# Optimization experiments

Measured on AMD Instinct MI355X. Metric: run time of the kernel, lower is better.

## Reference

```python
import jax, jax.numpy as jnp
import numpy as np

N_NODES = 100000

def _spmm(edge_index, edge_weight, support):
    # out[row] += w * support[col]  (COO spmm)
    row, col = edge_index[0], edge_index[1]
    msgs = edge_weight[:, None] * support[col]          # [E, D] gather
    return jax.ops.segment_sum(msgs, row, num_segments=N_NODES)

def setup_inputs() -> dict:
    key = jax.random.key(0)
    ks = jax.random.split(key, 7)
    N, E, F_IN, H1, H2 = N_NODES, 1600000, 256, 128, 64
    x = jax.random.normal(ks[0], (N, F_IN), dtype=jnp.float32)
    edge_index = jax.random.randint(ks[1], (2, E), 0, N, dtype=jnp.int64)
    edge_weight = jax.random.uniform(ks[2], (E,), dtype=jnp.float32)
    s1 = 1.0 / np.sqrt(H1)
    s2 = 1.0 / np.sqrt(H2)
    W1 = jax.random.uniform(ks[3], (F_IN, H1), jnp.float32, -s1, s1)
    b1 = jax.random.uniform(ks[4], (H1,), jnp.float32, -s1, s1)
    W2 = jax.random.uniform(ks[5], (H1, H2), jnp.float32, -s2, s2)
    b2 = jax.random.uniform(ks[6], (H2,), jnp.float32, -s2, s2)
    return {"x": x, "edge_index": edge_index, "edge_weight": edge_weight,
            "W1": W1, "b1": b1, "W2": W2, "b2": b2}

def reference(x, edge_index, edge_weight, W1, b1, W2, b2):
    # GraphConvolution 1: dense mm -> spmm -> bias, then ReLU
    h = _spmm(edge_index, edge_weight, x @ W1) + b1
    h = jax.nn.relu(h)
    # Dropout is identity in eval mode (training=False)
    # GraphConvolution 2
    out = _spmm(edge_index, edge_weight, h @ W2) + b2
    return out
```

## Files before the change

kernel.cpp:

```cpp
#include <hip/hip_runtime.h>


constexpr int F_IN = 256, H1 = 128, H2 = 64;
constexpr int BSH = 9;
constexpr int CHUNK = 8192;
constexpr float QS = 5.5f / 127.f;
constexpr float QSI = 127.f / 5.5f;

typedef __attribute__((ext_vector_type(8))) short bf16x8;
typedef __attribute__((ext_vector_type(8))) unsigned short u16x8;
typedef __attribute__((ext_vector_type(4))) float f32x4;

__device__ inline float bf2f(unsigned short u) { return __uint_as_float((unsigned)u << 16); }
__device__ inline unsigned short f2bf(float f) {
    unsigned u = __float_as_uint(f);
    u += 0x7fff + ((u >> 16) & 1);
    return (unsigned short)(u >> 16);
}

__device__ inline signed char f2i8(float f) {
    int q = __float2int_rn(f * QSI);
    q = q > 127 ? 127 : (q < -127 ? -127 : q);
    return (signed char)q;
}

__device__ inline void gload16(const void* g, void* l) {
    __builtin_amdgcn_global_load_lds((const __attribute__((address_space(1))) void*)g,
                                     (__attribute__((address_space(3))) void*)l, 16, 0, 0);
}

__global__ __launch_bounds__(256) void k_count(const int* __restrict__ ei, int E, int N,
                                               int* __restrict__ cnt, int NWG, int nbuck) {
    __shared__ int lh[256];
    int wg = blockIdx.x, t = threadIdx.x;
    if (t < nbuck) lh[t] = 0;
    __syncthreads();
    int base = wg * CHUNK;
#pragma unroll
    for (int j = 0; j < CHUNK / 1024; ++j) {
        int e = base + j * 1024 + t * 4;
        if (e + 3 < E) {
            int4 r4 = *(const int4*)&ei[e];
            unsigned r0 = (unsigned)r4.x, r1 = (unsigned)r4.y;
            unsigned r2 = (unsigned)r4.z, r3 = (unsigned)r4.w;
            if (r0 < (unsigned)N) atomicAdd(&lh[r0 >> BSH], 1);
            if (r1 < (unsigned)N) atomicAdd(&lh[r1 >> BSH], 1);
            if (r2 < (unsigned)N) atomicAdd(&lh[r2 >> BSH], 1);
            if (r3 < (unsigned)N) atomicAdd(&lh[r3 >> BSH], 1);
        } else {
            for (int k = 0; k < 4; ++k) {
                int ee = e + k;
                if (ee < E) {
                    unsigned r = (unsigned)ei[ee];
                    if (r < (unsigned)N) atomicAdd(&lh[r >> BSH], 1);
                }
            }
        }
    }
    __syncthreads();
    if (t < nbuck) cnt[t * NWG + wg] = lh[t];
}

__global__ __launch_bounds__(256) void k_rowscan(int* __restrict__ cnt, int NWG,
                                                 int* __restrict__ btot) {
    __shared__ int s[256];
    int b = blockIdx.x, t = threadIdx.x;
    int v = (t < NWG) ? cnt[b * NWG + t] : 0;
    s[t] = v;
    __syncthreads();
    for (int off = 1; off < 256; off <<= 1) {
        int tv = (t >= off) ? s[t - off] : 0;
        __syncthreads();
        s[t] += tv;
        __syncthreads();
    }
    if (t < NWG) cnt[b * NWG + t] = s[t] - v;
    if (t == 255) btot[b] = s[255];
}

__global__ __launch_bounds__(256) void k_bscan(const int* __restrict__ btot, int nbuck,
                                               int* __restrict__ bbase) {
    __shared__ int s[256];
    int t = threadIdx.x;
    int v = (t < nbuck) ? btot[t] : 0;
    s[t] = v;
    __syncthreads();
    for (int off = 1; off < 256; off <<= 1) {
        int tv = (t >= off) ? s[t - off] : 0;
        __syncthreads();
        s[t] += tv;
        __syncthreads();
    }
    if (t < nbuck) bbase[t] = s[t] - v;
    if (t == nbuck - 1) bbase[nbuck] = s[t];
}

__global__ __launch_bounds__(256) void k_place(const int* __restrict__ ei,
                                               const float* __restrict__ ew, int E, int N,
                                               const int* __restrict__ cnt,
                                               const int* __restrict__ bbase,
                                               int NWG, int nbuck,
                                               int2* __restrict__ tmp) {
    __shared__ int cur[256];
    int wg = blockIdx.x, t = threadIdx.x;
    if (t < nbuck) cur[t] = cnt[t * NWG + wg] + bbase[t];
    __syncthreads();
    int base = wg * CHUNK;
#pragma unroll
    for (int j = 0; j < CHUNK / 1024; ++j) {
        int e = base + j * 1024 + t * 4;
        if (e + 3 < E) {
            int4 r4 = *(const int4*)&ei[e];
            int4 c4 = *(const int4*)&ei[E + e];
            float4 w4 = *(const float4*)&ew[e];
            unsigned r, c;
            r = (unsigned)r4.x; c = (unsigned)c4.x;
            if (r < (unsigned)N && c < (unsigned)N) {
                int p = atomicAdd(&cur[r >> BSH], 1);
                tmp[p] = make_int2((int)(((r & 511u) << 17) | c), __float_as_int(w4.x));
            }
            r = (unsigned)r4.y; c = (unsigned)c4.y;
            if (r < (unsigned)N && c < (unsigned)N) {
                int p = atomicAdd(&cur[r >> BSH], 1);
                tmp[p] = make_int2((int)(((r & 511u) << 17) | c), __float_as_int(w4.y));
            }
            r = (unsigned)r4.z; c = (unsigned)c4.z;
            if (r < (unsigned)N && c < (unsigned)N) {
                int p = atomicAdd(&cur[r >> BSH], 1);
                tmp[p] = make_int2((int)(((r & 511u) << 17) | c), __float_as_int(w4.z));
            }
            r = (unsigned)r4.w; c = (unsigned)c4.w;
            if (r < (unsigned)N && c < (unsigned)N) {
                int p = atomicAdd(&cur[r >> BSH], 1);
                tmp[p] = make_int2((int)(((r & 511u) << 17) | c), __float_as_int(w4.w));
            }
        } else {
            for (int k = 0; k < 4; ++k) {
                int ee = e + k;
                if (ee < E) {
                    unsigned r = (unsigned)ei[ee];
                    unsigned c = (unsigned)ei[E + ee];
                    if (r < (unsigned)N && c < (unsigned)N) {
                        int p = atomicAdd(&cur[r >> BSH], 1);
                        tmp[p] = make_int2((int)(((r & 511u) << 17) | c),
                                           __float_as_int(ew[ee]));
                    }
                }
            }
        }
    }
}

__global__ __launch_bounds__(1024) void k_bfinal(const int2* __restrict__ tmp,
                                                 const int* __restrict__ bbase,
                                                 int* __restrict__ row_ptr,
                                                 int2* __restrict__ cw, int N, int nbuck) {
    __shared__ int hist[512], incl[512], cur[512];
    int b = blockIdx.x, t = threadIdx.x;
    int start = bbase[b];
    int end = bbase[b + 1];
    if (t < 512) hist[t] = 0;
    __syncthreads();
    for (int i = start + t; i < end; i += 1024)
        atomicAdd(&hist[(unsigned)tmp[i].x >> 17], 1);
    __syncthreads();
    if (t < 512) incl[t] = hist[t];
    __syncthreads();
    for (int off = 1; off < 512; off <<= 1) {
        int v = (t < 512 && t >= off) ? incl[t - off] : 0;
        __syncthreads();
        if (t < 512) incl[t] += v;
        __syncthreads();
    }
    int r0 = b << BSH;
    if (t < 512) {
        int abs_excl = start + incl[t] - hist[t];
        cur[t] = abs_excl;
        if (r0 + t < N) row_ptr[r0 + t] = abs_excl;
    }
    if (b == nbuck - 1 && t == 0) row_ptr[N] = end;
    __syncthreads();
    for (int i = start + t; i < end; i += 1024) {
        int2 e = tmp[i];
        int rl = (unsigned)e.x >> 17;
        int c = e.x & 0x1FFFF;
        int p = atomicAdd(&cur[rl], 1);
        cw[p] = make_int2(c << 7, e.y);
    }
}

__global__ __launch_bounds__(256) void k_prep_w(const float* __restrict__ W1,
                                                const float* __restrict__ W2,
                                                unsigned short* __restrict__ W1img,
                                                unsigned short* __restrict__ W2img) {
    int i = blockIdx.x * 256 + threadIdx.x;
    if (i < 32768) {
        int c = i >> 13, rem = i & 8191, nr = rem >> 6, gj = rem & 63;
        int gp = gj >> 3, j = gj & 7;
        int k = c * 64 + ((gp ^ (nr & 7)) << 3) + j;
        W1img[i] = f2bf(W1[k * H1 + nr]);
    } else if (i < 40960) {
        int i2 = i - 32768;
        int c = i2 >> 12, rem = i2 & 4095, nr = rem >> 6, gj = rem & 63;
        int gp = gj >> 3, j = gj & 7;
        int k = c * 64 + ((gp ^ (nr & 7)) << 3) + j;
        W2img[i2] = f2bf(W2[k * H2 + nr]);
    }
}

__global__ __launch_bounds__(512) void k_gemm1(const float* __restrict__ x,
                                               const unsigned short* __restrict__ Bimg,
                                               signed char* __restrict__ C, int M) {
    __shared__ unsigned short lB[32768];
    const int t = threadIdx.x, lane = t & 63, wid = t >> 6;
    const long row0 = (long)blockIdx.x * 128 + wid * 16;
    const int rl = lane & 15;
    const int g4 = lane >> 4;

#pragma unroll
    for (int rd = 0; rd < 8; ++rd)
        gload16(Bimg + rd * 4096 + wid * 512 + lane * 8,
                &lB[rd * 4096 + wid * 512]);

    f32x4 acc[8];
#pragma unroll
    for (int ni = 0; ni < 8; ++ni) acc[ni] = (f32x4){0.f, 0.f, 0.f, 0.f};

    const long arow = row0 + rl;
    const bool aok = arow < M;
    const float* xr = x + (aok ? arow : (long)(M - 1)) * F_IN + g4 * 8;

    float4 buf[2][4];
    buf[0][0] = *(const float4*)(xr + 0);
    buf[0][1] = *(const float4*)(xr + 4);
    buf[0][2] = *(const float4*)(xr + 32);
    buf[0][3] = *(const float4*)(xr + 36);

    __syncthreads();

#pragma unroll
    for (int c = 0; c < 4; ++c) {
        if (c < 3) {
            const float* xn = xr + (c + 1) * 64;
            buf[(c + 1) & 1][0] = *(const float4*)(xn + 0);
            buf[(c + 1) & 1][1] = *(const float4*)(xn + 4);
            buf[(c + 1) & 1][2] = *(const float4*)(xn + 32);
            buf[(c + 1) & 1][3] = *(const float4*)(xn + 36);
        }
#pragma unroll
        for (int kk = 0; kk < 2; ++kk) {
            const int g = kk * 4 + g4;
            float4 fa0 = buf[c & 1][kk * 2];
            float4 fa1 = buf[c & 1][kk * 2 + 1];
            bf16x8 b[8];
#pragma unroll
            for (int ni = 0; ni < 8; ++ni) {
                int nr = ni * 16 + rl;
                b[ni] = *(const bf16x8*)&lB[c * 8192 + nr * 64 + ((g ^ (nr & 7)) << 3)];
            }
            u16x8 ua;
            ua[0] = f2bf(fa0.x); ua[1] = f2bf(fa0.y);
            ua[2] = f2bf(fa0.z); ua[3] = f2bf(fa0.w);
            ua[4] = f2bf(fa1.x); ua[5] = f2bf(fa1.y);
            ua[6] = f2bf(fa1.z); ua[7] = f2bf(fa1.w);
            if (!aok) ua = (u16x8)0;
            bf16x8 a = *(bf16x8*)&ua;
#pragma unroll
            for (int ni = 0; ni < 8; ++ni)
                acc[ni] = __builtin_amdgcn_mfma_f32_16x16x32_bf16(a, b[ni], acc[ni], 0, 0, 0);
        }
    }
#pragma unroll
    for (int ni = 0; ni < 8; ++ni)
#pragma unroll
        for (int j = 0; j < 4; ++j) {
            long gr = row0 + g4 * 4 + j;
            int gc = ni * 16 + rl;
            if (gr < M) C[gr * H1 + gc] = f2i8(acc[ni][j]);
        }
}

__global__ __launch_bounds__(256) void k_gemm2(const unsigned short* __restrict__ Aimg,
                                               const unsigned short* __restrict__ Bimg,
                                               unsigned short* __restrict__ C, int M) {
    __shared__ unsigned short lA[64 * 64];
    __shared__ unsigned short lB[64 * 64];
    const int t = threadIdx.x, lane = t & 63, w = t >> 6;
    const int wm = w >> 1, wn = w & 1;
    const long tile = blockIdx.x;
    const long row0 = tile * 64;

    f32x4 acc[2][2];
#pragma unroll
    for (int mi = 0; mi < 2; ++mi)
#pragma unroll
        for (int ni = 0; ni < 2; ++ni) acc[mi][ni] = (f32x4){0.f, 0.f, 0.f, 0.f};

    for (int c = 0; c < 2; ++c) {
#pragma unroll
        for (int rd = 0; rd < 2; ++rd) {
            gload16(Aimg + (tile * 2 + c) * 4096 + rd * 2048 + w * 512 + lane * 8,
                    &lA[rd * 2048 + w * 512]);
            gload16(Bimg + c * 4096 + rd * 2048 + w * 512 + lane * 8,
                    &lB[rd * 2048 + w * 512]);
        }
        __syncthreads();
#pragma unroll
        for (int kk = 0; kk < 2; ++kk) {
            int g = kk * 4 + (lane >> 4);
            bf16x8 a[2], b[2];
#pragma unroll
            for (int mi = 0; mi < 2; ++mi) {
                int row = wm * 32 + mi * 16 + (lane & 15);
                a[mi] = *(const bf16x8*)&lA[row * 64 + ((g ^ (row & 7)) << 3)];
            }
#pragma unroll
            for (int ni = 0; ni < 2; ++ni) {
                int nr = wn * 32 + ni * 16 + (lane & 15);
                b[ni] = *(const bf16x8*)&lB[nr * 64 + ((g ^ (nr & 7)) << 3)];
            }
#pragma unroll
            for (int mi = 0; mi < 2; ++mi)
#pragma unroll
                for (int ni = 0; ni < 2; ++ni)
                    acc[mi][ni] = __builtin_amdgcn_mfma_f32_16x16x32_bf16(a[mi], b[ni],
                                                                          acc[mi][ni], 0, 0, 0);
        }
        __syncthreads();
    }
#pragma unroll
    for (int mi = 0; mi < 2; ++mi)
#pragma unroll
        for (int ni = 0; ni < 2; ++ni)
#pragma unroll
            for (int j = 0; j < 4; ++j) {
                long gr = row0 + wm * 32 + mi * 16 + (lane >> 4) * 4 + j;
                int gc = wn * 32 + ni * 16 + (lane & 15);
                if (gr < M) C[gr * H2 + gc] = f2bf(acc[mi][ni][j]);
            }
}

__global__ __launch_bounds__(256) void k_spmm1(const int* __restrict__ row_ptr,
                                               const int2* __restrict__ cw,
                                               const signed char* __restrict__ sup,
                                               const float* __restrict__ bias,
                                               unsigned int* __restrict__ himg, int n) {
    int wave = (blockIdx.x * 256 + threadIdx.x) >> 6;
    int half = (threadIdx.x >> 5) & 1;
    int l = threadIdx.x & 31;
    int row = wave * 2 + half;
    if (row >= n) return;
    int s = row_ptr[row], e = row_ptr[row + 1];
    const char* base = (const char*)sup + (l << 2);
    float a0 = 0.f, a1 = 0.f, a2 = 0.f, a3 = 0.f;
    int i = s;
    for (; i + 8 <= e; i += 8) {
        int2 e0 = cw[i], e1 = cw[i + 1], e2 = cw[i + 2], e3 = cw[i + 3];
        int2 e4 = cw[i + 4], e5 = cw[i + 5], e6 = cw[i + 6], e7 = cw[i + 7];
        unsigned v0 = *(const unsigned*)(base + e0.x);
        unsigned v1 = *(const unsigned*)(base + e1.x);
        unsigned v2 = *(const unsigned*)(base + e2.x);
        unsigned v3 = *(const unsigned*)(base + e3.x);
        unsigned v4 = *(const unsigned*)(base + e4.x);
        unsigned v5 = *(const unsigned*)(base + e5.x);
        unsigned v6 = *(const unsigned*)(base + e6.x);
        unsigned v7 = *(const unsigned*)(base + e7.x);
        float w0 = __int_as_float(e0.y), w1 = __int_as_float(e1.y);
        float w2 = __int_as_float(e2.y), w3 = __int_as_float(e3.y);
        float w4 = __int_as_float(e4.y), w5 = __int_as_float(e5.y);
        float w6 = __int_as_float(e6.y), w7 = __int_as_float(e7.y);
        a0 += w0 * (float)(signed char)(v0);
        a1 += w0 * (float)(signed char)(v0 >> 8);
        a2 += w0 * (float)(signed char)(v0 >> 16);
        a3 += w0 * (float)((int)v0 >> 24);
        a0 += w1 * (float)(signed char)(v1);
        a1 += w1 * (float)(signed char)(v1 >> 8);
        a2 += w1 * (float)(signed char)(v1 >> 16);
        a3 += w1 * (float)((int)v1 >> 24);
        a0 += w2 * (float)(signed char)(v2);
        a1 += w2 * (float)(signed char)(v2 >> 8);
        a2 += w2 * (float)(signed char)(v2 >> 16);
        a3 += w2 * (float)((int)v2 >> 24);
        a0 += w3 * (float)(signed char)(v3);
        a1 += w3 * (float)(signed char)(v3 >> 8);
        a2 += w3 * (float)(signed char)(v3 >> 16);
        a3 += w3 * (float)((int)v3 >> 24);
        a0 += w4 * (float)(signed char)(v4);
        a1 += w4 * (float)(signed char)(v4 >> 8);
        a2 += w4 * (float)(signed char)(v4 >> 16);
        a3 += w4 * (float)((int)v4 >> 24);
        a0 += w5 * (float)(signed char)(v5);
        a1 += w5 * (float)(signed char)(v5 >> 8);
        a2 += w5 * (float)(signed char)(v5 >> 16);
        a3 += w5 * (float)((int)v5 >> 24);
        a0 += w6 * (float)(signed char)(v6);
        a1 += w6 * (float)(signed char)(v6 >> 8);
        a2 += w6 * (float)(signed char)(v6 >> 16);
        a3 += w6 * (float)((int)v6 >> 24);
        a0 += w7 * (float)(signed char)(v7);
        a1 += w7 * (float)(signed char)(v7 >> 8);
        a2 += w7 * (float)(signed char)(v7 >> 16);
        a3 += w7 * (float)((int)v7 >> 24);
    }
    for (; i + 4 <= e; i += 4) {
        int2 e0 = cw[i], e1 = cw[i + 1], e2 = cw[i + 2], e3 = cw[i + 3];
        unsigned v0 = *(const unsigned*)(base + e0.x);
        unsigned v1 = *(const unsigned*)(base + e1.x);
        unsigned v2 = *(const unsigned*)(base + e2.x);
        unsigned v3 = *(const unsigned*)(base + e3.x);
        float w0 = __int_as_float(e0.y), w1 = __int_as_float(e1.y);
        float w2 = __int_as_float(e2.y), w3 = __int_as_float(e3.y);
        a0 += w0 * (float)(signed char)(v0);
        a1 += w0 * (float)(signed char)(v0 >> 8);
        a2 += w0 * (float)(signed char)(v0 >> 16);
        a3 += w0 * (float)((int)v0 >> 24);
        a0 += w1 * (float)(signed char)(v1);
        a1 += w1 * (float)(signed char)(v1 >> 8);
        a2 += w1 * (float)(signed char)(v1 >> 16);
        a3 += w1 * (float)((int)v1 >> 24);
        a0 += w2 * (float)(signed char)(v2);
        a1 += w2 * (float)(signed char)(v2 >> 8);
        a2 += w2 * (float)(signed char)(v2 >> 16);
        a3 += w2 * (float)((int)v2 >> 24);
        a0 += w3 * (float)(signed char)(v3);
        a1 += w3 * (float)(signed char)(v3 >> 8);
        a2 += w3 * (float)(signed char)(v3 >> 16);
        a3 += w3 * (float)((int)v3 >> 24);
    }
    for (; i < e; ++i) {
        int2 ee = cw[i];
        unsigned v = *(const unsigned*)(base + ee.x);
        float w = __int_as_float(ee.y);
        a0 += w * (float)(signed char)(v);
        a1 += w * (float)(signed char)(v >> 8);
        a2 += w * (float)(signed char)(v >> 16);
        a3 += w * (float)((int)v >> 24);
    }
    float4 b = *(const float4*)&bias[l * 4];
    float o0 = fmaxf(fmaf(a0, QS, b.x), 0.f);
    float o1 = fmaxf(fmaf(a1, QS, b.y), 0.f);
    float o2 = fmaxf(fmaf(a2, QS, b.z), 0.f);
    float o3 = fmaxf(fmaf(a3, QS, b.w), 0.f);
    int tile = row >> 6, r = row & 63;
    int p = l * 2;
    unsigned pixw = (unsigned)((tile * 2 + (p >> 5)) * 2048 + r * 32 +
                               ((((p & 31) >> 2) ^ (r & 7)) << 2) + (p & 3));
    uint2 val;
    val.x = (unsigned)f2bf(o0) | ((unsigned)f2bf(o1) << 16);
    val.y = (unsigned)f2bf(o2) | ((unsigned)f2bf(o3) << 16);
    *(uint2*)&himg[pixw] = val;
}

__global__ __launch_bounds__(256) void k_spmm2(const int* __restrict__ row_ptr,
                                               const int2* __restrict__ cw,
                                               const unsigned short* __restrict__ sup2,
                                               const float* __restrict__ bias,
                                               float* __restrict__ out, int n) {
    int wave = (blockIdx.x * 256 + threadIdx.x) >> 6;
    int half = (threadIdx.x >> 5) & 1;
    int l = threadIdx.x & 31;
    int row = wave * 2 + half;
    if (row >= n) return;
    int s = row_ptr[row], e = row_ptr[row + 1];
    const char* base = (const char*)sup2 + (l << 2);
    float a0 = 0.f, a1 = 0.f;
    int i = s;
    for (; i + 8 <= e; i += 8) {
        int2 e0 = cw[i], e1 = cw[i + 1], e2 = cw[i + 2], e3 = cw[i + 3];
        int2 e4 = cw[i + 4], e5 = cw[i + 5], e6 = cw[i + 6], e7 = cw[i + 7];
        unsigned v0 = *(const unsigned*)(base + e0.x);
        unsigned v1 = *(const unsigned*)(base + e1.x);
        unsigned v2 = *(const unsigned*)(base + e2.x);
        unsigned v3 = *(const unsigned*)(base + e3.x);
        unsigned v4 = *(const unsigned*)(base + e4.x);
        unsigned v5 = *(const unsigned*)(base + e5.x);
        unsigned v6 = *(const unsigned*)(base + e6.x);
        unsigned v7 = *(const unsigned*)(base + e7.x);
        float w0 = __int_as_float(e0.y), w1 = __int_as_float(e1.y);
        float w2 = __int_as_float(e2.y), w3 = __int_as_float(e3.y);
        float w4 = __int_as_float(e4.y), w5 = __int_as_float(e5.y);
        float w6 = __int_as_float(e6.y), w7 = __int_as_float(e7.y);
        a0 += w0 * __uint_as_float(v0 << 16);
        a1 += w0 * __uint_as_float(v0 & 0xffff0000u);
        a0 += w1 * __uint_as_float(v1 << 16);
        a1 += w1 * __uint_as_float(v1 & 0xffff0000u);
        a0 += w2 * __uint_as_float(v2 << 16);
        a1 += w2 * __uint_as_float(v2 & 0xffff0000u);
        a0 += w3 * __uint_as_float(v3 << 16);
        a1 += w3 * __uint_as_float(v3 & 0xffff0000u);
        a0 += w4 * __uint_as_float(v4 << 16);
        a1 += w4 * __uint_as_float(v4 & 0xffff0000u);
        a0 += w5 * __uint_as_float(v5 << 16);
        a1 += w5 * __uint_as_float(v5 & 0xffff0000u);
        a0 += w6 * __uint_as_float(v6 << 16);
        a1 += w6 * __uint_as_float(v6 & 0xffff0000u);
        a0 += w7 * __uint_as_float(v7 << 16);
        a1 += w7 * __uint_as_float(v7 & 0xffff0000u);
    }
    for (; i + 4 <= e; i += 4) {
        int2 e0 = cw[i], e1 = cw[i + 1], e2 = cw[i + 2], e3 = cw[i + 3];
        unsigned v0 = *(const unsigned*)(base + e0.x);
        unsigned v1 = *(const unsigned*)(base + e1.x);
        unsigned v2 = *(const unsigned*)(base + e2.x);
        unsigned v3 = *(const unsigned*)(base + e3.x);
        float w0 = __int_as_float(e0.y), w1 = __int_as_float(e1.y);
        float w2 = __int_as_float(e2.y), w3 = __int_as_float(e3.y);
        a0 += w0 * __uint_as_float(v0 << 16);
        a1 += w0 * __uint_as_float(v0 & 0xffff0000u);
        a0 += w1 * __uint_as_float(v1 << 16);
        a1 += w1 * __uint_as_float(v1 & 0xffff0000u);
        a0 += w2 * __uint_as_float(v2 << 16);
        a1 += w2 * __uint_as_float(v2 & 0xffff0000u);
        a0 += w3 * __uint_as_float(v3 << 16);
        a1 += w3 * __uint_as_float(v3 & 0xffff0000u);
    }
    for (; i < e; ++i) {
        int2 ee = cw[i];
        unsigned v = *(const unsigned*)(base + ee.x);
        float w = __int_as_float(ee.y);
        a0 += w * __uint_as_float(v << 16);
        a1 += w * __uint_as_float(v & 0xffff0000u);
    }
    float2 b = *(const float2*)&bias[l * 2];
    *(float2*)&out[(long)row * H2 + l * 2] = make_float2(a0 + b.x, a1 + b.y);
}


extern "C" void kernel_launch(void* const* d_in, const int* in_sizes, int n_in,
                              void* d_out, int out_size, void* d_ws, size_t ws_size,
                              hipStream_t stream) {
    (void)n_in; (void)out_size; (void)ws_size;
    const float* x = (const float*)d_in[0];
    const int* ei = (const int*)d_in[1];
    const float* ew = (const float*)d_in[2];
    const float* W1 = (const float*)d_in[3];
    const float* b1 = (const float*)d_in[4];
    const float* W2 = (const float*)d_in[5];
    const float* b2 = (const float*)d_in[6];
    float* out = (float*)d_out;

    const int E = in_sizes[2];
    const int N = in_sizes[0] / F_IN;
    const int nbuck = (N + (1 << BSH) - 1) >> BSH;
    const int NWG = (E + CHUNK - 1) / CHUNK;
    const int ntile = (N + 63) / 64;
    const int ng1 = (N + 127) / 128;
    const int gSp = (N + 7) / 8;

    size_t off = 0;
    auto take = [&off](size_t bytes) { size_t p = off; off = (off + bytes + 255) & ~(size_t)255; return p; };
    size_t o_sup    = take((size_t)N * H1);
    size_t o_himg   = take((size_t)ntile * 2 * 4096 * 2);
    size_t o_w1img  = take((size_t)4 * 128 * 64 * 2);
    size_t o_w2img  = take((size_t)2 * 64 * 64 * 2);
    size_t o_rowptr = take(((size_t)N + 1) * 4);
    size_t o_cnt    = take((size_t)256 * 256 * 4);
    size_t o_btot   = take(256 * 4);
    size_t o_bbase  = take(260 * 4);
    size_t o_cw     = take((size_t)E * 8);

    char* wsb = (char*)d_ws;
    signed char*    sup   = (signed char*)(wsb + o_sup);
    unsigned int*   himg  = (unsigned int*)(wsb + o_himg);
    unsigned short* W1img = (unsigned short*)(wsb + o_w1img);
    unsigned short* W2img = (unsigned short*)(wsb + o_w2img);
    int* row_ptr = (int*)(wsb + o_rowptr);
    int* cnt     = (int*)(wsb + o_cnt);
    int* btot    = (int*)(wsb + o_btot);
    int* bbase   = (int*)(wsb + o_bbase);
    int2* tmp    = (int2*)(wsb + o_himg);
    int2* cw     = (int2*)(wsb + o_cw);

    k_count<<<NWG, 256, 0, stream>>>(ei, E, N, cnt, NWG, nbuck);
    k_rowscan<<<nbuck, 256, 0, stream>>>(cnt, NWG, btot);
    k_bscan<<<1, 256, 0, stream>>>(btot, nbuck, bbase);
    k_place<<<NWG, 256, 0, stream>>>(ei, ew, E, N, cnt, bbase, NWG, nbuck, tmp);
    k_bfinal<<<nbuck, 1024, 0, stream>>>(tmp, bbase, row_ptr, cw, N, nbuck);

    k_prep_w<<<160, 256, 0, stream>>>(W1, W2, W1img, W2img);

    k_gemm1<<<ng1, 512, 0, stream>>>(x, W1img, sup, N);
    k_spmm1<<<gSp, 256, 0, stream>>>(row_ptr, cw, sup, b1, himg, N);
    k_gemm2<<<ntile, 256, 0, stream>>>((const unsigned short*)himg, W2img,
                                       (unsigned short*)sup, N);
    k_spmm2<<<gSp, 256, 0, stream>>>(row_ptr, cw, (const unsigned short*)sup,
                                     b2, out, N);
}
```

Measured before the change: 159.7 us.

## Fuse edge bucket counting with first GEMM into one heterogeneous launch

Merges the edge-histogram kernel and the x@W1 GEMM into a single launch. The first NWG blocks do the bucket count and the remaining blocks each compute a 64-row by 64-column half tile. The GEMM tile shrinks from 128x128 with 512 threads to 64x64 with 256 threads, so each block uses less LDS and more blocks can be resident. The aim is to overlap the latency-bound counting pass with the bandwidth-bound GEMM and to drop one launch. In exchange, each row of x is now read twice, once per column half, and the fp32-to-bf16 conversion moves to the library intrinsic.

```diff
diff --git a/kernel.cpp b/kernel.cpp
--- a/kernel.cpp
+++ b/kernel.cpp
@@ -1,4 +1,5 @@
 #include <hip/hip_runtime.h>
+#include <hip/hip_bf16.h>
 
 
 constexpr int F_IN = 256, H1 = 128, H2 = 64;
@@ -18,6 +19,13 @@
     return (unsigned short)(u >> 16);
 }
 
+__device__ inline unsigned short hf2bf(float f) {
+    __hip_bfloat16 b = __float2bfloat16(f);
+    unsigned short u;
+    __builtin_memcpy(&u, &b, 2);
+    return u;
+}
+
 __device__ inline signed char f2i8(float f) {
     int q = __float2int_rn(f * QSI);
     q = q > 127 ? 127 : (q < -127 ? -127 : q);
@@ -29,36 +37,116 @@
                                      (__attribute__((address_space(3))) void*)l, 16, 0, 0);
 }
 
-__global__ __launch_bounds__(256) void k_count(const int* __restrict__ ei, int E, int N,
-                                               int* __restrict__ cnt, int NWG, int nbuck) {
-    __shared__ int lh[256];
-    int wg = blockIdx.x, t = threadIdx.x;
-    if (t < nbuck) lh[t] = 0;
-    __syncthreads();
-    int base = wg * CHUNK;
-#pragma unroll
-    for (int j = 0; j < CHUNK / 1024; ++j) {
-        int e = base + j * 1024 + t * 4;
-        if (e + 3 < E) {
-            int4 r4 = *(const int4*)&ei[e];
-            unsigned r0 = (unsigned)r4.x, r1 = (unsigned)r4.y;
-            unsigned r2 = (unsigned)r4.z, r3 = (unsigned)r4.w;
-            if (r0 < (unsigned)N) atomicAdd(&lh[r0 >> BSH], 1);
-            if (r1 < (unsigned)N) atomicAdd(&lh[r1 >> BSH], 1);
-            if (r2 < (unsigned)N) atomicAdd(&lh[r2 >> BSH], 1);
-            if (r3 < (unsigned)N) atomicAdd(&lh[r3 >> BSH], 1);
-        } else {
-            for (int k = 0; k < 4; ++k) {
-                int ee = e + k;
-                if (ee < E) {
-                    unsigned r = (unsigned)ei[ee];
-                    if (r < (unsigned)N) atomicAdd(&lh[r >> BSH], 1);
+__global__ __launch_bounds__(256) void k_g1c(const float* __restrict__ x,
+                                             const unsigned short* __restrict__ Bimg,
+                                             signed char* __restrict__ C, int M,
+                                             const int* __restrict__ ei, int E, int N,
+                                             int* __restrict__ cnt, int NWG, int nbuck) {
+    __shared__ unsigned short lB[16384];
+    const int t = threadIdx.x;
+
+    if ((int)blockIdx.x < NWG) {
+        int* lh = (int*)lB;
+        int wg = blockIdx.x;
+        if (t < nbuck) lh[t] = 0;
+        __syncthreads();
+        int base = wg * CHUNK;
+#pragma unroll
+        for (int j = 0; j < CHUNK / 1024; ++j) {
+            int e = base + j * 1024 + t * 4;
+            if (e + 3 < E) {
+                int4 r4 = *(const int4*)&ei[e];
+                unsigned r0 = (unsigned)r4.x, r1 = (unsigned)r4.y;
+                unsigned r2 = (unsigned)r4.z, r3 = (unsigned)r4.w;
+                if (r0 < (unsigned)N) atomicAdd(&lh[r0 >> BSH], 1);
+                if (r1 < (unsigned)N) atomicAdd(&lh[r1 >> BSH], 1);
+                if (r2 < (unsigned)N) atomicAdd(&lh[r2 >> BSH], 1);
+                if (r3 < (unsigned)N) atomicAdd(&lh[r3 >> BSH], 1);
+            } else {
+                for (int k = 0; k < 4; ++k) {
+                    int ee = e + k;
+                    if (ee < E) {
+                        unsigned r = (unsigned)ei[ee];
+                        if (r < (unsigned)N) atomicAdd(&lh[r >> BSH], 1);
+                    }
                 }
             }
         }
-    }
-    __syncthreads();
-    if (t < nbuck) cnt[t * NWG + wg] = lh[t];
+        __syncthreads();
+        if (t < nbuck) cnt[t * NWG + wg] = lh[t];
+        return;
+    }
+
+    const int bid = blockIdx.x - NWG;
+    const int tile = bid >> 1, h = bid & 1;
+    const int lane = t & 63, wid = t >> 6;
+    const long row0 = (long)tile * 64 + wid * 16;
+    const int rl = lane & 15;
+    const int g4 = lane >> 4;
+
+#pragma unroll
+    for (int rd = 0; rd < 8; ++rd) {
+        int c = rd >> 1, hp = rd & 1;
+        gload16(Bimg + c * 8192 + h * 4096 + hp * 2048 + t * 8,
+                &lB[c * 4096 + hp * 2048 + t * 8]);
+    }
+
+    f32x4 acc[4];
+#pragma unroll
+    for (int ni = 0; ni < 4; ++ni) acc[ni] = (f32x4){0.f, 0.f, 0.f, 0.f};
+
+    const long arow = row0 + rl;
+    const bool aok = arow < M;
+    const float* xr = x + (aok ? arow : (long)(M - 1)) * F_IN + g4 * 8;
+
+    float4 buf[2][4];
+    buf[0][0] = *(const float4*)(xr + 0);
+    buf[0][1] = *(const float4*)(xr + 4);
+    buf[0][2] = *(const float4*)(xr + 32);
+    buf[0][3] = *(const float4*)(xr + 36);
+
+    __syncthreads();
+
+#pragma unroll
+    for (int c = 0; c < 4; ++c) {
+        if (c < 3) {
+            const float* xn = xr + (c + 1) * 64;
+            buf[(c + 1) & 1][0] = *(const float4*)(xn + 0);
+            buf[(c + 1) & 1][1] = *(const float4*)(xn + 4);
+            buf[(c + 1) & 1][2] = *(const float4*)(xn + 32);
+            buf[(c + 1) & 1][3] = *(const float4*)(xn + 36);
+        }
+#pragma unroll
+        for (int kk = 0; kk < 2; ++kk) {
+            const int g = kk * 4 + g4;
+            float4 fa0 = buf[c & 1][kk * 2];
+            float4 fa1 = buf[c & 1][kk * 2 + 1];
+            bf16x8 b[4];
+#pragma unroll
+            for (int ni = 0; ni < 4; ++ni) {
+                int nl = ni * 16 + rl;
+                b[ni] = *(const bf16x8*)&lB[c * 4096 + nl * 64 + ((g ^ (nl & 7)) << 3)];
+            }
+            u16x8 ua;
+            ua[0] = hf2bf(fa0.x); ua[1] = hf2bf(fa0.y);
+            ua[2] = hf2bf(fa0.z); ua[3] = hf2bf(fa0.w);
+            ua[4] = hf2bf(fa1.x); ua[5] = hf2bf(fa1.y);
+            ua[6] = hf2bf(fa1.z); ua[7] = hf2bf(fa1.w);
+            if (!aok) ua = (u16x8)0;
+            bf16x8 a = *(bf16x8*)&ua;
+#pragma unroll
+            for (int ni = 0; ni < 4; ++ni)
+                acc[ni] = __builtin_amdgcn_mfma_f32_16x16x32_bf16(a, b[ni], acc[ni], 0, 0, 0);
+        }
+    }
+#pragma unroll
+    for (int ni = 0; ni < 4; ++ni)
+#pragma unroll
+        for (int j = 0; j < 4; ++j) {
+            long gr = row0 + g4 * 4 + j;
+            int gc = h * 64 + ni * 16 + rl;
+            if (gr < M) C[gr * H1 + gc] = f2i8(acc[ni][j]);
+        }
 }
 
 __global__ __launch_bounds__(256) void k_rowscan(int* __restrict__ cnt, int NWG,
@@ -206,78 +294,6 @@
         int k = c * 64 + ((gp ^ (nr & 7)) << 3) + j;
         W2img[i2] = f2bf(W2[k * H2 + nr]);
     }
-}
-
-__global__ __launch_bounds__(512) void k_gemm1(const float* __restrict__ x,
-                                               const unsigned short* __restrict__ Bimg,
-                                               signed char* __restrict__ C, int M) {
-    __shared__ unsigned short lB[32768];
-    const int t = threadIdx.x, lane = t & 63, wid = t >> 6;
-    const long row0 = (long)blockIdx.x * 128 + wid * 16;
-    const int rl = lane & 15;
-    const int g4 = lane >> 4;
-
-#pragma unroll
-    for (int rd = 0; rd < 8; ++rd)
-        gload16(Bimg + rd * 4096 + wid * 512 + lane * 8,
-                &lB[rd * 4096 + wid * 512]);
-
-    f32x4 acc[8];
-#pragma unroll
-    for (int ni = 0; ni < 8; ++ni) acc[ni] = (f32x4){0.f, 0.f, 0.f, 0.f};
-
-    const long arow = row0 + rl;
-    const bool aok = arow < M;
-    const float* xr = x + (aok ? arow : (long)(M - 1)) * F_IN + g4 * 8;
-
-    float4 buf[2][4];
-    buf[0][0] = *(const float4*)(xr + 0);
-    buf[0][1] = *(const float4*)(xr + 4);
-    buf[0][2] = *(const float4*)(xr + 32);
-    buf[0][3] = *(const float4*)(xr + 36);
-
-    __syncthreads();
-
-#pragma unroll
-    for (int c = 0; c < 4; ++c) {
-        if (c < 3) {
-            const float* xn = xr + (c + 1) * 64;
-            buf[(c + 1) & 1][0] = *(const float4*)(xn + 0);
-            buf[(c + 1) & 1][1] = *(const float4*)(xn + 4);
-            buf[(c + 1) & 1][2] = *(const float4*)(xn + 32);
-            buf[(c + 1) & 1][3] = *(const float4*)(xn + 36);
-        }
-#pragma unroll
-        for (int kk = 0; kk < 2; ++kk) {
-            const int g = kk * 4 + g4;
-            float4 fa0 = buf[c & 1][kk * 2];
-            float4 fa1 = buf[c & 1][kk * 2 + 1];
-            bf16x8 b[8];
-#pragma unroll
-            for (int ni = 0; ni < 8; ++ni) {
-                int nr = ni * 16 + rl;
-                b[ni] = *(const bf16x8*)&lB[c * 8192 + nr * 64 + ((g ^ (nr & 7)) << 3)];
-            }
-            u16x8 ua;
-            ua[0] = f2bf(fa0.x); ua[1] = f2bf(fa0.y);
-            ua[2] = f2bf(fa0.z); ua[3] = f2bf(fa0.w);
-            ua[4] = f2bf(fa1.x); ua[5] = f2bf(fa1.y);
-            ua[6] = f2bf(fa1.z); ua[7] = f2bf(fa1.w);
-            if (!aok) ua = (u16x8)0;
-            bf16x8 a = *(bf16x8*)&ua;
-#pragma unroll
-            for (int ni = 0; ni < 8; ++ni)
-                acc[ni] = __builtin_amdgcn_mfma_f32_16x16x32_bf16(a, b[ni], acc[ni], 0, 0, 0);
-        }
-    }
-#pragma unroll
-    for (int ni = 0; ni < 8; ++ni)
-#pragma unroll
-        for (int j = 0; j < 4; ++j) {
-            long gr = row0 + g4 * 4 + j;
-            int gc = ni * 16 + rl;
-            if (gr < M) C[gr * H1 + gc] = f2i8(acc[ni][j]);
-        }
 }
 
 __global__ __launch_bounds__(256) void k_gemm2(const unsigned short* __restrict__ Aimg,
@@ -544,7 +560,6 @@
     const int nbuck = (N + (1 << BSH) - 1) >> BSH;
     const int NWG = (E + CHUNK - 1) / CHUNK;
     const int ntile = (N + 63) / 64;
-    const int ng1 = (N + 127) / 128;
     const int gSp = (N + 7) / 8;
 
     size_t off = 0;
@@ -571,15 +586,15 @@
     int2* tmp    = (int2*)(wsb + o_himg);
     int2* cw     = (int2*)(wsb + o_cw);
 
-    k_count<<<NWG, 256, 0, stream>>>(ei, E, N, cnt, NWG, nbuck);
+    k_prep_w<<<160, 256, 0, stream>>>(W1, W2, W1img, W2img);
+
+    k_g1c<<<NWG + 2 * ntile, 256, 0, stream>>>(x, W1img, sup, N, ei, E, N, cnt, NWG, nbuck);
+
     k_rowscan<<<nbuck, 256, 0, stream>>>(cnt, NWG, btot);
     k_bscan<<<1, 256, 0, stream>>>(btot, nbuck, bbase);
     k_place<<<NWG, 256, 0, stream>>>(ei, ew, E, N, cnt, bbase, NWG, nbuck, tmp);
     k_bfinal<<<nbuck, 1024, 0, stream>>>(tmp, bbase, row_ptr, cw, N, nbuck);
 
-    k_prep_w<<<160, 256, 0, stream>>>(W1, W2, W1img, W2img);
-
-    k_gemm1<<<ng1, 512, 0, stream>>>(x, W1img, sup, N);
     k_spmm1<<<gSp, 256, 0, stream>>>(row_ptr, cw, sup, b1, himg, N);
     k_gemm2<<<ntile, 256, 0, stream>>>((const unsigned short*)himg, W2img,
                                        (unsigned short*)sup, N);
```

After: 168.6 us. 1.06x slower.
